# Performance work log

Hardware: AMD Instinct MI355X
Metric: run time of the kernel (lower is better)

Reference implementation:

```python
import jax, jax.numpy as jnp
from jax import lax
import numpy as np

B, T, D, H, OUT = 2048, 512, 1, 50, 3


def setup_inputs() -> dict:
    key = jax.random.key(0)
    ks = jax.random.split(key, 7)
    s = 1.0 / np.sqrt(H)  # PyTorch LSTM init scale
    x = jax.random.normal(ks[0], (B, T, D), dtype=jnp.float32)
    W_ih = jax.random.uniform(ks[1], (4 * H, D), minval=-s, maxval=s, dtype=jnp.float32)
    W_hh = jax.random.uniform(ks[2], (4 * H, H), minval=-s, maxval=s, dtype=jnp.float32)
    b_ih = jax.random.uniform(ks[3], (4 * H,), minval=-s, maxval=s, dtype=jnp.float32)
    b_hh = jax.random.uniform(ks[4], (4 * H,), minval=-s, maxval=s, dtype=jnp.float32)
    fc_w = jax.random.uniform(ks[5], (OUT, H), minval=-s, maxval=s, dtype=jnp.float32)
    fc_b = jax.random.uniform(ks[6], (OUT,), minval=-s, maxval=s, dtype=jnp.float32)
    return {"x": x, "W_ih": W_ih, "W_hh": W_hh, "b_ih": b_ih, "b_hh": b_hh,
            "fc_w": fc_w, "fc_b": fc_b}


def reference(x, W_ih, W_hh, b_ih, b_hh, fc_w, fc_b):
    # x: [B, T, 1]; PyTorch gate order: i, f, g, o
    b = x.shape[0]
    h = H
    # Precompute input projection for all timesteps: [B, T, 4H]
    x_proj = jnp.einsum('btd,gd->btg', x, W_ih) + b_ih + b_hh

    def step(carry, xp_t):
        h_t, c_t = carry
        gates = xp_t + h_t @ W_hh.T  # [B, 4H]
        i = jax.nn.sigmoid(gates[:, 0 * h:1 * h])
        f = jax.nn.sigmoid(gates[:, 1 * h:2 * h])
        g = jnp.tanh(gates[:, 2 * h:3 * h])
        o = jax.nn.sigmoid(gates[:, 3 * h:4 * h])
        c_new = f * c_t + i * g
        h_new = o * jnp.tanh(c_new)
        return (h_new, c_new), None

    h0 = jnp.zeros((b, h), dtype=x.dtype)
    c0 = jnp.zeros((b, h), dtype=x.dtype)
    (h_T, _), _ = lax.scan(step, (h0, c0), jnp.swapaxes(x_proj, 0, 1))
    # fc on last timestep hidden state only (out[:, -1, :])
    return h_T @ fc_w.T + fc_b
```

## Files before the change

### kernel.cpp

```cpp
#include <hip/hip_runtime.h>


#define BB 2048
#define TT 512
#define HH 50
#define NB 16
#define NW 16
#define XP 513
#define HS 72
#define LO_SCALE  2048.0f
#define LO_ISCALE 0.00048828125f
#define L1 -1.4426950408889634f
#define L2 -2.8853900817779268f

typedef __attribute__((ext_vector_type(4))) float    f32x4;
typedef __attribute__((ext_vector_type(8))) _Float16 f16x8;

__global__ __launch_bounds__(NW * 64)
void lstm_r15_kernel(const float* __restrict__ x,
                     const float* __restrict__ W_ih,
                     const float* __restrict__ W_hh,
                     const float* __restrict__ b_ih,
                     const float* __restrict__ b_hh,
                     const float* __restrict__ fc_w,
                     const float* __restrict__ fc_b,
                     float* __restrict__ out) {
    __shared__ float xs[NB * XP];
    __shared__ __align__(16) unsigned short hf[2][NB][HS];
    __shared__ float hfin[NB][64];

    const int tid  = threadIdx.x;
    const int w    = tid >> 6;
    const int lane = tid & 63;
    const int hi   = lane >> 4;
    const int bcol = lane & 15;
    const int b0   = blockIdx.x * NB;

    for (int idx = tid; idx < NB * TT; idx += NW * 64) {
        xs[(idx >> 9) * XP + (idx & 511)] = x[(b0 + (idx >> 9)) * TT + (idx & 511)];
    }
    if (tid < NB) xs[tid * XP + 512] = 0.0f;
    for (int idx = tid; idx < (int)(sizeof(hf) / 4); idx += NW * 64) {
        ((unsigned*)hf)[idx] = 0;
    }

    const int ga = bcol & 3;
    const int ua = 4 * w + (bcol >> 2);
    const bool ok = (ua < HH);
    const float Lg = (ga == 2) ? L2 : L1;
    f16x8 Ah0, Ah1, Al0, Al1;
    #pragma unroll
    for (int s = 0; s < 2; ++s) {
        #pragma unroll
        for (int e = 0; e < 8; ++e) {
            const int k = 32 * s + 8 * hi + e;
            _Float16 ah = (_Float16)0.0f, al = (_Float16)0.0f;
            if (ok) {
                if (k < HH) {
                    const float wv = Lg * W_hh[(ga * HH + ua) * HH + k];
                    ah = (_Float16)wv;
                    al = (_Float16)((wv - (float)ah) * LO_SCALE);
                } else if (k == 61) {
                    al = (_Float16)(Lg * W_ih[ga * HH + ua]);
                } else if (k == 62) {
                    const float bv = Lg * (b_ih[ga * HH + ua] + b_hh[ga * HH + ua]);
                    ah = (_Float16)bv;
                    al = (_Float16)((bv - (float)ah) * LO_SCALE);
                } else if (k == 63) {
                    const float wv = Lg * W_ih[ga * HH + ua];
                    ah = (_Float16)wv;
                    al = (_Float16)((wv - (float)ah) * LO_SCALE);
                }
            }
            if (s == 0) { Ah0[e] = ah; Al0[e] = al; }
            else        { Ah1[e] = ah; Al1[e] = al; }
        }
    }

    const unsigned short* rb  = &hf[0][bcol][8 * hi];
    unsigned short*       wb  = &hf[0][bcol][4 * w + hi];
    unsigned short*       xwb = &hf[0][bcol][0];
    const bool xwriter = (w == 15) && (hi == 3);
    const bool hwriter = (4 * w + hi) < HH;

    __syncthreads();

    if (xwriter) {
        const unsigned short one_h = __builtin_bit_cast(unsigned short, (_Float16)1.0f);
        xwb[62] = one_h;
        xwb[1152 + 62] = one_h;
        const float x0 = xs[bcol * XP + 0];
        const _Float16 xh = (_Float16)x0;
        const _Float16 xl = (_Float16)((x0 - (float)xh) * LO_SCALE);
        xwb[63] = __builtin_bit_cast(unsigned short, xh);
        xwb[61] = __builtin_bit_cast(unsigned short, xl);
    }

    float c = 0.0f, hcur = 0.0f;
    const f32x4 zero4 = {0.0f, 0.0f, 0.0f, 0.0f};

    __syncthreads();

#define STEP(CB, T) { \
        const f16x8 B0 = *(const f16x8*)(rb + (CB) * 1152); \
        const f16x8 B1 = *(const f16x8*)(rb + (CB) * 1152 + 32); \
        f32x4 acc  = __builtin_amdgcn_mfma_f32_16x16x32_f16(Ah0, B0, zero4, 0, 0, 0); \
        f32x4 acc2 = __builtin_amdgcn_mfma_f32_16x16x32_f16(Al0, B0, zero4, 0, 0, 0); \
        acc  = __builtin_amdgcn_mfma_f32_16x16x32_f16(Ah1, B1, acc,  0, 0, 0); \
        acc2 = __builtin_amdgcn_mfma_f32_16x16x32_f16(Al1, B1, acc2, 0, 0, 0); \
         \
        const float v0 = fmaf(acc2[0], LO_ISCALE, acc[0]); \
        const float v1 = fmaf(acc2[1], LO_ISCALE, acc[1]); \
        const float v2 = fmaf(acc2[2], LO_ISCALE, acc[2]); \
        const float v3 = fmaf(acc2[3], LO_ISCALE, acc[3]); \
        const float E1 = __builtin_amdgcn_exp2f(v0);    \
        const float E2 = __builtin_amdgcn_exp2f(v1);    \
        const float G  = __builtin_amdgcn_exp2f(v2);    \
        const float E4 = __builtin_amdgcn_exp2f(v3);    \
        const float P1 = 1.0f + E1, P2 = 1.0f + E2; \
        const float PG = 1.0f + G,  P4 = 1.0f + E4; \
        const float MG = 1.0f - G; \
        const float N  = fmaf(c * P1, PG, MG * P2); \
        const float D  = (P1 * P2) * PG; \
        c = N * __builtin_amdgcn_rcpf(D); \
        const float C5 = __builtin_amdgcn_exp2f(L2 * c); \
        const float Q  = (1.0f + C5) * P4; \
        hcur = (1.0f - C5) * __builtin_amdgcn_rcpf(Q); \
        if (hwriter) \
            wb[(1 - (CB)) * 1152] = __builtin_bit_cast(unsigned short, (_Float16)hcur); \
        if (xwriter) { \
            const float xn = xs[bcol * XP + (T) + 1]; \
            const _Float16 xh = (_Float16)xn; \
            const _Float16 xl = (_Float16)((xn - (float)xh) * LO_SCALE); \
            xwb[(1 - (CB)) * 1152 + 63] = __builtin_bit_cast(unsigned short, xh); \
            xwb[(1 - (CB)) * 1152 + 61] = __builtin_bit_cast(unsigned short, xl); \
        } \
        __syncthreads(); }

    #pragma unroll 1
    for (int t = 0; t < TT; t += 2) {
        STEP(0, t)
        STEP(1, t + 1)
    }
#undef STEP

    hfin[bcol][4 * w + hi] = hcur;
    __syncthreads();
    if (tid < NB * 3) {
        const int b = tid / 3, o = tid % 3;
        float s = fc_b[o];
        for (int uu = 0; uu < HH; ++uu)
            s = fmaf(hfin[b][uu], fc_w[o * HH + uu], s);
        out[(b0 + b) * 3 + o] = s;
    }
}

extern "C" void kernel_launch(void* const* d_in, const int* in_sizes, int n_in,
                              void* d_out, int out_size, void* d_ws, size_t ws_size,
                              hipStream_t stream) {
    const float* x    = (const float*)d_in[0];
    const float* W_ih = (const float*)d_in[1];
    const float* W_hh = (const float*)d_in[2];
    const float* b_ih = (const float*)d_in[3];
    const float* b_hh = (const float*)d_in[4];
    const float* fc_w = (const float*)d_in[5];
    const float* fc_b = (const float*)d_in[6];
    float* out = (float*)d_out;

    dim3 grid(BB / NB);
    dim3 block(NW * 64);
    lstm_r15_kernel<<<grid, block, 0, stream>>>(x, W_ih, W_hh, b_ih, b_hh,
                                                fc_w, fc_b, out);
}
```

Before: 276.9 us.

## Drop fp16 hi/lo weight split and fold bias into MFMA accumulator init

Removes the low-order fp16 compensation matrices, so each step issues two MFMAs instead of four and skips the hi/lo recombination FMAs. The combined bias now seeds the MFMA accumulator in fp32 instead of riding in the B operand, and x keeps its hi/lo split through a pre-scaled W_ih column written with one vector store. This shortens the per-step critical path of the serial recurrence, but W_hh is now rounded to plain fp16, which costs accuracy over 512 steps.

```diff
diff --git a/kernel.cpp b/kernel.cpp
--- a/kernel.cpp
+++ b/kernel.cpp
@@ -8,16 +8,17 @@
 #define NW 16
 #define XP 513
 #define HS 72
-#define LO_SCALE  2048.0f
-#define LO_ISCALE 0.00048828125f
+#define XSC   32.0f
+#define XSCI  0.03125f
 #define L1 -1.4426950408889634f
 #define L2 -2.8853900817779268f
 
-typedef __attribute__((ext_vector_type(4))) float    f32x4;
-typedef __attribute__((ext_vector_type(8))) _Float16 f16x8;
+typedef __attribute__((ext_vector_type(4))) float          f32x4;
+typedef __attribute__((ext_vector_type(8))) _Float16       f16x8;
+typedef __attribute__((ext_vector_type(4))) unsigned short u16x4;
 
 __global__ __launch_bounds__(NW * 64)
-void lstm_r15_kernel(const float* __restrict__ x,
+void lstm_r16_kernel(const float* __restrict__ x,
                      const float* __restrict__ W_ih,
                      const float* __restrict__ W_hh,
                      const float* __restrict__ b_ih,
@@ -48,33 +49,32 @@
     const int ua = 4 * w + (bcol >> 2);
     const bool ok = (ua < HH);
     const float Lg = (ga == 2) ? L2 : L1;
-    f16x8 Ah0, Ah1, Al0, Al1;
+    f16x8 Ah0, Ah1;
     #pragma unroll
     for (int s = 0; s < 2; ++s) {
         #pragma unroll
         for (int e = 0; e < 8; ++e) {
             const int k = 32 * s + 8 * hi + e;
-            _Float16 ah = (_Float16)0.0f, al = (_Float16)0.0f;
+            _Float16 ah = (_Float16)0.0f;
             if (ok) {
                 if (k < HH) {
-                    const float wv = Lg * W_hh[(ga * HH + ua) * HH + k];
-                    ah = (_Float16)wv;
-                    al = (_Float16)((wv - (float)ah) * LO_SCALE);
+                    ah = (_Float16)(Lg * W_hh[(ga * HH + ua) * HH + k]);
                 } else if (k == 61) {
-                    al = (_Float16)(Lg * W_ih[ga * HH + ua]);
-                } else if (k == 62) {
-                    const float bv = Lg * (b_ih[ga * HH + ua] + b_hh[ga * HH + ua]);
-                    ah = (_Float16)bv;
-                    al = (_Float16)((bv - (float)ah) * LO_SCALE);
+                    ah = (_Float16)(Lg * W_ih[ga * HH + ua] * XSCI);
                 } else if (k == 63) {
-                    const float wv = Lg * W_ih[ga * HH + ua];
-                    ah = (_Float16)wv;
-                    al = (_Float16)((wv - (float)ah) * LO_SCALE);
+                    ah = (_Float16)(Lg * W_ih[ga * HH + ua]);
                 }
             }
-            if (s == 0) { Ah0[e] = ah; Al0[e] = al; }
-            else        { Ah1[e] = ah; Al1[e] = al; }
+            if (s == 0) Ah0[e] = ah; else Ah1[e] = ah;
         }
+    }
+
+    f32x4 bias_c;
+    #pragma unroll
+    for (int r = 0; r < 4; ++r) {
+        const int u = 4 * w + hi;
+        const float Lr = (r == 2) ? L2 : L1;
+        bias_c[r] = (u < HH) ? Lr * (b_ih[r * HH + u] + b_hh[r * HH + u]) : 0.0f;
     }
 
     const unsigned short* rb  = &hf[0][bcol][8 * hi];
@@ -86,37 +86,27 @@
     __syncthreads();
 
     if (xwriter) {
-        const unsigned short one_h = __builtin_bit_cast(unsigned short, (_Float16)1.0f);
-        xwb[62] = one_h;
-        xwb[1152 + 62] = one_h;
         const float x0 = xs[bcol * XP + 0];
         const _Float16 xh = (_Float16)x0;
-        const _Float16 xl = (_Float16)((x0 - (float)xh) * LO_SCALE);
-        xwb[63] = __builtin_bit_cast(unsigned short, xh);
-        xwb[61] = __builtin_bit_cast(unsigned short, xl);
+        const _Float16 xl = (_Float16)((x0 - (float)xh) * XSC);
+        u16x4 P = {0, __builtin_bit_cast(unsigned short, xl), 0,
+                      __builtin_bit_cast(unsigned short, xh)};
+        *(u16x4*)(xwb + 60) = P;
     }
 
     float c = 0.0f, hcur = 0.0f;
-    const f32x4 zero4 = {0.0f, 0.0f, 0.0f, 0.0f};
 
     __syncthreads();
 
 #define STEP(CB, T) { \
         const f16x8 B0 = *(const f16x8*)(rb + (CB) * 1152); \
         const f16x8 B1 = *(const f16x8*)(rb + (CB) * 1152 + 32); \
-        f32x4 acc  = __builtin_amdgcn_mfma_f32_16x16x32_f16(Ah0, B0, zero4, 0, 0, 0); \
-        f32x4 acc2 = __builtin_amdgcn_mfma_f32_16x16x32_f16(Al0, B0, zero4, 0, 0, 0); \
-        acc  = __builtin_amdgcn_mfma_f32_16x16x32_f16(Ah1, B1, acc,  0, 0, 0); \
-        acc2 = __builtin_amdgcn_mfma_f32_16x16x32_f16(Al1, B1, acc2, 0, 0, 0); \
-         \
-        const float v0 = fmaf(acc2[0], LO_ISCALE, acc[0]); \
-        const float v1 = fmaf(acc2[1], LO_ISCALE, acc[1]); \
-        const float v2 = fmaf(acc2[2], LO_ISCALE, acc[2]); \
-        const float v3 = fmaf(acc2[3], LO_ISCALE, acc[3]); \
-        const float E1 = __builtin_amdgcn_exp2f(v0);    \
-        const float E2 = __builtin_amdgcn_exp2f(v1);    \
-        const float G  = __builtin_amdgcn_exp2f(v2);    \
-        const float E4 = __builtin_amdgcn_exp2f(v3);    \
+        f32x4 acc = __builtin_amdgcn_mfma_f32_16x16x32_f16(Ah0, B0, bias_c, 0, 0, 0); \
+        acc = __builtin_amdgcn_mfma_f32_16x16x32_f16(Ah1, B1, acc, 0, 0, 0); \
+        const float E1 = __builtin_amdgcn_exp2f(acc[0]);    \
+        const float E2 = __builtin_amdgcn_exp2f(acc[1]);    \
+        const float G  = __builtin_amdgcn_exp2f(acc[2]);    \
+        const float E4 = __builtin_amdgcn_exp2f(acc[3]);    \
         const float P1 = 1.0f + E1, P2 = 1.0f + E2; \
         const float PG = 1.0f + G,  P4 = 1.0f + E4; \
         const float MG = 1.0f - G; \
@@ -131,9 +121,10 @@
         if (xwriter) { \
             const float xn = xs[bcol * XP + (T) + 1]; \
             const _Float16 xh = (_Float16)xn; \
-            const _Float16 xl = (_Float16)((xn - (float)xh) * LO_SCALE); \
-            xwb[(1 - (CB)) * 1152 + 63] = __builtin_bit_cast(unsigned short, xh); \
-            xwb[(1 - (CB)) * 1152 + 61] = __builtin_bit_cast(unsigned short, xl); \
+            const _Float16 xl = (_Float16)((xn - (float)xh) * XSC); \
+            u16x4 P = {0, __builtin_bit_cast(unsigned short, xl), 0, \
+                          __builtin_bit_cast(unsigned short, xh)}; \
+            *(u16x4*)(xwb + (1 - (CB)) * 1152 + 60) = P; \
         } \
         __syncthreads(); }
 
@@ -169,6 +160,6 @@
 
     dim3 grid(BB / NB);
     dim3 block(NW * 64);
-    lstm_r15_kernel<<<grid, block, 0, stream>>>(x, W_ih, W_hh, b_ih, b_hh,
+    lstm_r16_kernel<<<grid, block, 0, stream>>>(x, W_ih, W_hh, b_ih, b_hh,
                                                 fc_w, fc_b, out);
 }
```

New measurement: 262.0 us. 1.06x faster.
